# Performance work log

Measured on AMD Instinct MI355X. Metric: run time of the kernel, lower is better.

Reference implementation:

```python
import jax, jax.numpy as jnp
import numpy as np

B, S, D_IN, D_H = 4, 2048, 1024, 1024

def setup_inputs() -> dict:
    key = jax.random.key(0)
    kx, kq, kk, kv = jax.random.split(key, 4)
    # nn.Linear default init: U(-1/sqrt(fan_in), 1/sqrt(fan_in)); stored as [out, in]
    bound = 1.0 / np.sqrt(D_IN)
    x = jax.random.normal(kx, (B, S, D_IN), dtype=jnp.float32)
    W_q = jax.random.uniform(kq, (D_H, D_IN), jnp.float32, -bound, bound)
    W_k = jax.random.uniform(kk, (D_H, D_IN), jnp.float32, -bound, bound)
    W_v = jax.random.uniform(kv, (D_H, D_IN), jnp.float32, -bound, bound)
    return {"x": x, "W_q": W_q, "W_k": W_k, "W_v": W_v}

def reference(x, W_q, W_k, W_v):
    # Q = x @ W_q.T, etc. (nn.Linear with bias=False)
    Q = jnp.einsum('bsd,hd->bsh', x, W_q)
    K = jnp.einsum('bsd,hd->bsh', x, W_k)
    V = jnp.einsum('bsd,hd->bsh', x, W_v)
    # NOTE: original scales by sqrt(Q.shape[1]) == sqrt(seq_len), not sqrt(d)
    scale = 1.0 / jnp.sqrt(jnp.asarray(Q.shape[1], Q.dtype))
    scores = jnp.einsum('bqh,bkh->bqk', Q, K) * scale  # [B,S,S]
    attn = jax.nn.softmax(scores, axis=-1)
    return jnp.einsum('bqk,bkh->bqh', attn, V)
```

## Files before the change

kernel.cpp:

```cpp
#include <hip/hip_runtime.h>

typedef unsigned short ushort_t;
typedef __attribute__((ext_vector_type(8))) __bf16 bf16x8;
typedef __attribute__((ext_vector_type(4))) float floatx4;

__device__ __forceinline__ ushort_t f2bf(float f) {
    unsigned int u = __builtin_bit_cast(unsigned int, f);
    u = (u + 0x7fffu + ((u >> 16) & 1u)) >> 16;
    return (ushort_t)u;
}

__device__ __forceinline__ int sw(int row, int cg) {
    return ((row << 2) + ((cg ^ row ^ (row >> 2)) & 3)) << 3;
}

template <int BM, int BN, int IM, int IN>
__device__ __forceinline__ void gemm_core_pf(
    const ushort_t* __restrict__ A, int lda,
    const ushort_t* __restrict__ B, int ldb,
    int K, int tile_m, int tile_n,
    ushort_t* As, ushort_t* Bs,
    floatx4 (&acc)[IM][IN]) {

    constexpr int SA = BM * 4 / 256;
    constexpr int SB = BN * 4 / 256;

    const int tid  = threadIdx.x;
    const int lane = tid & 63;
    const int wave = tid >> 6;
    const int wm   = wave >> 1, wn = wave & 1;
    const int quad = lane >> 4;
    const int l16  = lane & 15;

#pragma unroll
    for (int i = 0; i < IM; i++)
#pragma unroll
        for (int j = 0; j < IN; j++) acc[i][j] = (floatx4){0.f, 0.f, 0.f, 0.f};

    const ushort_t* ga[SA];
    int la[SA];
#pragma unroll
    for (int s = 0; s < SA; s++) {
        int seg = tid + s * 256;
        int r = seg >> 2, c = (seg ^ r ^ (r >> 2)) & 3;
        ga[s] = A + (long)(r + tile_m) * lda + c * 8;
        la[s] = seg * 8;
    }
    const ushort_t* gb[SB];
    int lb[SB];
#pragma unroll
    for (int s = 0; s < SB; s++) {
        int seg = tid + s * 256;
        int r = seg >> 2, c = (seg ^ r ^ (r >> 2)) & 3;
        gb[s] = B + (long)(r + tile_n) * ldb + c * 8;
        lb[s] = seg * 8;
    }

    const int nk = K >> 5;

    bf16x8 ra[SA], rb[SB];
#pragma unroll
    for (int s = 0; s < SA; s++) ra[s] = *(const bf16x8*)ga[s];
#pragma unroll
    for (int s = 0; s < SB; s++) rb[s] = *(const bf16x8*)gb[s];
#pragma unroll
    for (int s = 0; s < SA; s++) *(bf16x8*)&As[la[s]] = ra[s];
#pragma unroll
    for (int s = 0; s < SB; s++) *(bf16x8*)&Bs[lb[s]] = rb[s];
    __syncthreads();

    for (int ks = 0; ks < nk; ++ks) {
        const int cur = ks & 1, nxt = cur ^ 1;

        if (ks + 1 < nk) {
            const int k1 = (ks + 1) << 5;
#pragma unroll
            for (int s = 0; s < SA; s++) ra[s] = *(const bf16x8*)(ga[s] + k1);
#pragma unroll
            for (int s = 0; s < SB; s++) rb[s] = *(const bf16x8*)(gb[s] + k1);
        }

        const ushort_t* as = &As[cur * BM * 32];
        const ushort_t* bs = &Bs[cur * BN * 32];
        bf16x8 af[IM], bfr[IN];
#pragma unroll
        for (int im = 0; im < IM; im++)
            af[im] = *(const bf16x8*)&as[sw(wm * IM * 16 + im * 16 + l16, quad)];
#pragma unroll
        for (int in = 0; in < IN; in++)
            bfr[in] = *(const bf16x8*)&bs[sw(wn * IN * 16 + in * 16 + l16, quad)];
#pragma unroll
        for (int im = 0; im < IM; im++)
#pragma unroll
            for (int in = 0; in < IN; in++)
                acc[im][in] = __builtin_amdgcn_mfma_f32_16x16x32_bf16(
                    af[im], bfr[in], acc[im][in], 0, 0, 0);

        if (ks + 1 < nk) {
#pragma unroll
            for (int s = 0; s < SA; s++) *(bf16x8*)&As[nxt * BM * 32 + la[s]] = ra[s];
#pragma unroll
            for (int s = 0; s < SB; s++) *(bf16x8*)&Bs[nxt * BN * 32 + lb[s]] = rb[s];
            __syncthreads();
        }
    }
}

__global__ void cvt_kernel(const float* __restrict__ x,
                           const float* __restrict__ wv,
                           ushort_t* __restrict__ xb,
                           ushort_t* __restrict__ wvb,
                           float* __restrict__ lsum) {
    const int bx = blockIdx.x;
    if (bx >= 9216) {
        int idx = (bx - 9216) * 256 + threadIdx.x;
        ((float4*)lsum)[idx] = (float4){0.f, 0.f, 0.f, 0.f};
        return;
    }
    const float* src;
    ushort_t* dst;
    long g;
    if (bx < 8192) { src = x;  dst = xb;  g = ((long)bx * 256 + threadIdx.x) * 4; }
    else           { src = wv; dst = wvb; g = ((long)(bx - 8192) * 256 + threadIdx.x) * 4; }
    float4 v = *(const float4*)(src + g);
    ushort4 o;
    o.x = f2bf(v.x); o.y = f2bf(v.y); o.z = f2bf(v.z); o.w = f2bf(v.w);
    *(ushort4*)(dst + g) = o;
}

__global__ void tkern(const float* __restrict__ wq, const float* __restrict__ wk,
                      ushort_t* __restrict__ wqT, ushort_t* __restrict__ wkT) {
    const float* src = blockIdx.z ? wk : wq;
    ushort_t* dst = blockIdx.z ? wkT : wqT;
    __shared__ ushort_t tile[64 * 80];

    const int t = threadIdx.x;
    const int h0 = blockIdx.y * 64, d0 = blockIdx.x * 64;
    {
        int i = t >> 2, cg = (t & 3) << 4;
        const float4* p = (const float4*)(src + (long)(h0 + i) * 1024 + d0 + cg);
#pragma unroll
        for (int k = 0; k < 4; k++) {
            float4 v = p[k];
            ushort_t* q = &tile[i * 80 + cg + k * 4];
            q[0] = f2bf(v.x); q[1] = f2bf(v.y); q[2] = f2bf(v.z); q[3] = f2bf(v.w);
        }
    }
    __syncthreads();
    {
        int j = t >> 2, ig = (t & 3) << 4;
        ushort_t tmp[16];
#pragma unroll
        for (int k = 0; k < 16; k++) tmp[k] = tile[(ig + k) * 80 + j];
        ushort_t* o = dst + (long)(d0 + j) * 1024 + h0 + ig;
        *(uint4*)o = ((uint4*)tmp)[0];
        *(uint4*)(o + 8) = ((uint4*)tmp)[1];
    }
}

__global__ __launch_bounds__(256) void ggemm_kernel(
    const ushort_t* __restrict__ wkT, const ushort_t* __restrict__ wqT,
    ushort_t* __restrict__ G) {
    __shared__ __align__(16) ushort_t As[2 * 64 * 32];
    __shared__ __align__(16) ushort_t Bs[2 * 64 * 32];
    const int tile_m = blockIdx.y * 64, tile_n = blockIdx.x * 64;
    floatx4 acc[2][2];
    gemm_core_pf<64, 64, 2, 2>(wkT, 1024, wqT, 1024, 1024, tile_m, tile_n, As, Bs, acc);
    const int lane = threadIdx.x & 63, wave = threadIdx.x >> 6;
    const int wm = wave >> 1, wn = wave & 1, quad = lane >> 4, l16 = lane & 15;
#pragma unroll
    for (int im = 0; im < 2; im++)
#pragma unroll
        for (int r = 0; r < 4; r++) {
            int row = tile_m + wm * 32 + im * 16 + quad * 4 + r;
#pragma unroll
            for (int in = 0; in < 2; in++) {
                int col = tile_n + wn * 32 + in * 16 + l16;
                G[(long)row * 1024 + col] = f2bf(acc[im][in][r]);
            }
        }
}

__global__ __launch_bounds__(256) void yv_kernel(
    const ushort_t* __restrict__ xb,
    const ushort_t* __restrict__ Gb,
    const ushort_t* __restrict__ wvb,
    ushort_t* __restrict__ Yb,
    ushort_t* __restrict__ VTb) {

    __shared__ __align__(16) ushort_t As[2 * 128 * 32];
    __shared__ __align__(16) ushort_t Bs[2 * 128 * 32];

    const int z = blockIdx.z;
    const ushort_t *A, *B;
    ushort_t* C;
    int ldc, tile_m, tile_n;
    if (z == 0) {
        A = xb; B = Gb; C = Yb; ldc = 1024;
        tile_m = blockIdx.y * 128; tile_n = blockIdx.x * 128;
    } else {
        A = wvb; B = xb; C = VTb; ldc = 8192;
        tile_m = blockIdx.x * 128; tile_n = blockIdx.y * 128;
    }

    floatx4 acc[4][4];
    gemm_core_pf<128, 128, 4, 4>(A, 1024, B, 1024, 1024, tile_m, tile_n, As, Bs, acc);

    const int lane = threadIdx.x & 63, wave = threadIdx.x >> 6;
    const int wm = wave >> 1, wn = wave & 1, quad = lane >> 4, l16 = lane & 15;
#pragma unroll
    for (int im = 0; im < 4; im++)
#pragma unroll
        for (int r = 0; r < 4; r++) {
            int row = tile_m + wm * 64 + im * 16 + quad * 4 + r;
#pragma unroll
            for (int in = 0; in < 4; in++) {
                int col = tile_n + wn * 64 + in * 16 + l16;
                C[(long)row * ldc + col] = f2bf(acc[im][in][r]);
            }
        }
}

__global__ __launch_bounds__(256) void pexp_kernel(
    const ushort_t* __restrict__ Yb,
    const ushort_t* __restrict__ xb,
    ushort_t* __restrict__ Pb,
    float* __restrict__ lsum) {

    __shared__ __align__(16) ushort_t As[2 * 128 * 32];
    __shared__ __align__(16) ushort_t Bs[2 * 128 * 32];

    const int z = blockIdx.z;
    const ushort_t* A = Yb + (long)z * 2097152;
    const ushort_t* B = xb + (long)z * 2097152;
    ushort_t* C = Pb + (long)z * 4194304;
    float* l = lsum + z * 2048;
    const int tile_m = blockIdx.y * 128;
    const int tile_n = blockIdx.x * 128;

    floatx4 acc[4][4];
    gemm_core_pf<128, 128, 4, 4>(A, 1024, B, 1024, 1024, tile_m, tile_n, As, Bs, acc);

    const float scale = 0.022097086912079608f;
    const int lane = threadIdx.x & 63, wave = threadIdx.x >> 6;
    const int wm = wave >> 1, wn = wave & 1, quad = lane >> 4, l16 = lane & 15;
#pragma unroll
    for (int im = 0; im < 4; im++)
#pragma unroll
        for (int r = 0; r < 4; r++) {
            int row = tile_m + wm * 64 + im * 16 + quad * 4 + r;
            float psum = 0.f;
#pragma unroll
            for (int in = 0; in < 4; in++) {
                int col = tile_n + wn * 64 + in * 16 + l16;
                float e = __expf(acc[im][in][r] * scale);
                C[(long)row * 2048 + col] = f2bf(e);
                psum += e;
            }
            psum += __shfl_xor(psum, 1, 64);
            psum += __shfl_xor(psum, 2, 64);
            psum += __shfl_xor(psum, 4, 64);
            psum += __shfl_xor(psum, 8, 64);
            if (l16 == 0) atomicAdd(&l[row], psum);
        }
}

__global__ __launch_bounds__(256) void out_kernel(
    const ushort_t* __restrict__ Pb,
    const ushort_t* __restrict__ VTb,
    float* __restrict__ out,
    const float* __restrict__ lsum) {

    __shared__ __align__(16) ushort_t As[2 * 128 * 32];
    __shared__ __align__(16) ushort_t Bs[2 * 128 * 32];

    const int z = blockIdx.z;
    const ushort_t* A = Pb + (long)z * 4194304;
    const ushort_t* B = VTb + (long)z * 2048;
    float* C = out + (long)z * 2097152;
    const float* l = lsum + z * 2048;
    const int tile_m = blockIdx.y * 128;
    const int tile_n = blockIdx.x * 128;

    floatx4 acc[4][4];
    gemm_core_pf<128, 128, 4, 4>(A, 2048, B, 8192, 2048, tile_m, tile_n, As, Bs, acc);

    const int lane = threadIdx.x & 63, wave = threadIdx.x >> 6;
    const int wm = wave >> 1, wn = wave & 1, quad = lane >> 4, l16 = lane & 15;
#pragma unroll
    for (int im = 0; im < 4; im++)
#pragma unroll
        for (int r = 0; r < 4; r++) {
            int row = tile_m + wm * 64 + im * 16 + quad * 4 + r;
            float li = 1.0f / l[row];
#pragma unroll
            for (int in = 0; in < 4; in++) {
                int col = tile_n + wn * 64 + in * 16 + l16;
                C[(long)row * 1024 + col] = acc[im][in][r] * li;
            }
        }
}

extern "C" void kernel_launch(void* const* d_in, const int* in_sizes, int n_in,
                              void* d_out, int out_size, void* d_ws, size_t ws_size,
                              hipStream_t stream) {
    const float* x  = (const float*)d_in[0];
    const float* wq = (const float*)d_in[1];
    const float* wk = (const float*)d_in[2];
    const float* wv = (const float*)d_in[3];

    ushort_t* xb  = (ushort_t*)d_ws;
    ushort_t* wvb = xb  + 8388608;
    ushort_t* wqT = wvb + 1048576;
    ushort_t* wkT = wqT + 1048576;
    ushort_t* Gb  = wkT + 1048576;
    ushort_t* Yb  = Gb  + 1048576;
    ushort_t* VTb = Yb  + 8388608;
    ushort_t* Pb  = VTb + 8388608;
    float*    lsum = (float*)(Pb + 16777216);
    float*    out  = (float*)d_out;

    cvt_kernel<<<9224, 256, 0, stream>>>(x, wv, xb, wvb, lsum);

    tkern<<<dim3(16, 16, 2), 256, 0, stream>>>(wq, wk, wqT, wkT);

    ggemm_kernel<<<dim3(16, 16), 256, 0, stream>>>(wkT, wqT, Gb);

    yv_kernel<<<dim3(8, 64, 2), 256, 0, stream>>>(xb, Gb, wvb, Yb, VTb);

    pexp_kernel<<<dim3(16, 16, 4), 256, 0, stream>>>(Yb, xb, Pb, lsum);

    out_kernel<<<dim3(8, 16, 4), 256, 0, stream>>>(Pb, VTb, out, lsum);
}
```

Measured before the change: 269.8 us.

## Use async global-to-LDS loads with triple-buffered pipeline in GEMM core

Replaces the register-staged double-buffered GEMM main loop with direct global_load_lds async copies into a three-slot shared buffer, prefetching two k-steps ahead. The wait on outstanding loads uses explicit vmcnt counts plus a barrier. The aim is to remove the register round trip and the VGPRs used for staging, and to hide more load latency. In exchange it uses more LDS per block (48KB for the 128-tile kernels), which may lower occupancy. It also depends on hand-tuned vmcnt counts being correct.

```diff
diff --git a/kernel.cpp b/kernel.cpp
--- a/kernel.cpp
+++ b/kernel.cpp
@@ -10,20 +10,29 @@
     return (ushort_t)u;
 }
 
+__device__ __forceinline__ void async16(const ushort_t* g, ushort_t* l) {
+    __builtin_amdgcn_global_load_lds(
+        (const __attribute__((address_space(1))) unsigned int*)g,
+        (__attribute__((address_space(3))) unsigned int*)l,
+        16 , 0 , 0 );
+}
+
 __device__ __forceinline__ int sw(int row, int cg) {
     return ((row << 2) + ((cg ^ row ^ (row >> 2)) & 3)) << 3;
 }
 
 template <int BM, int BN, int IM, int IN>
-__device__ __forceinline__ void gemm_core_pf(
+__device__ __forceinline__ void gemm_core_p3(
     const ushort_t* __restrict__ A, int lda,
     const ushort_t* __restrict__ B, int ldb,
     int K, int tile_m, int tile_n,
-    ushort_t* As, ushort_t* Bs,
+    ushort_t* buf,
     floatx4 (&acc)[IM][IN]) {
 
     constexpr int SA = BM * 4 / 256;
     constexpr int SB = BN * 4 / 256;
+    constexpr int SLOT = (BM + BN) * 32;
+    constexpr int BOFF = BM * 32;
 
     const int tid  = threadIdx.x;
     const int lane = tid & 63;
@@ -53,35 +62,43 @@
         int seg = tid + s * 256;
         int r = seg >> 2, c = (seg ^ r ^ (r >> 2)) & 3;
         gb[s] = B + (long)(r + tile_n) * ldb + c * 8;
-        lb[s] = seg * 8;
+        lb[s] = BOFF + seg * 8;
     }
 
     const int nk = K >> 5;
 
-    bf16x8 ra[SA], rb[SB];
-#pragma unroll
-    for (int s = 0; s < SA; s++) ra[s] = *(const bf16x8*)ga[s];
-#pragma unroll
-    for (int s = 0; s < SB; s++) rb[s] = *(const bf16x8*)gb[s];
-#pragma unroll
-    for (int s = 0; s < SA; s++) *(bf16x8*)&As[la[s]] = ra[s];
-#pragma unroll
-    for (int s = 0; s < SB; s++) *(bf16x8*)&Bs[lb[s]] = rb[s];
-    __syncthreads();
-
-    for (int ks = 0; ks < nk; ++ks) {
-        const int cur = ks & 1, nxt = cur ^ 1;
-
-        if (ks + 1 < nk) {
-            const int k1 = (ks + 1) << 5;
-#pragma unroll
-            for (int s = 0; s < SA; s++) ra[s] = *(const bf16x8*)(ga[s] + k1);
-#pragma unroll
-            for (int s = 0; s < SB; s++) rb[s] = *(const bf16x8*)(gb[s] + k1);
-        }
-
-        const ushort_t* as = &As[cur * BM * 32];
-        const ushort_t* bs = &Bs[cur * BN * 32];
+#pragma unroll
+    for (int p = 0; p < 2; ++p) {
+#pragma unroll
+        for (int s = 0; s < SA; s++) async16(ga[s] + p * 32, buf + p * SLOT + la[s]);
+#pragma unroll
+        for (int s = 0; s < SB; s++) async16(gb[s] + p * 32, buf + p * SLOT + lb[s]);
+    }
+
+    int slot = 0, slot2 = 2;
+    for (int k = 0; k < nk; ++k) {
+        if (k + 1 < nk) {
+            if constexpr (SA + SB == 4)
+                asm volatile("s_waitcnt vmcnt(4)" ::: "memory");
+            else
+                asm volatile("s_waitcnt vmcnt(2)" ::: "memory");
+        } else {
+            asm volatile("s_waitcnt vmcnt(0)" ::: "memory");
+        }
+        __builtin_amdgcn_s_barrier();
+        asm volatile("" ::: "memory");
+
+        if (k + 2 < nk) {
+            const int koff = (k + 2) << 5;
+            ushort_t* dst = buf + slot2 * SLOT;
+#pragma unroll
+            for (int s = 0; s < SA; s++) async16(ga[s] + koff, dst + la[s]);
+#pragma unroll
+            for (int s = 0; s < SB; s++) async16(gb[s] + koff, dst + lb[s]);
+        }
+
+        const ushort_t* as = buf + slot * SLOT;
+        const ushort_t* bs = as + BOFF;
         bf16x8 af[IM], bfr[IN];
 #pragma unroll
         for (int im = 0; im < IM; im++)
@@ -96,13 +113,8 @@
                 acc[im][in] = __builtin_amdgcn_mfma_f32_16x16x32_bf16(
                     af[im], bfr[in], acc[im][in], 0, 0, 0);
 
-        if (ks + 1 < nk) {
-#pragma unroll
-            for (int s = 0; s < SA; s++) *(bf16x8*)&As[nxt * BM * 32 + la[s]] = ra[s];
-#pragma unroll
-            for (int s = 0; s < SB; s++) *(bf16x8*)&Bs[nxt * BN * 32 + lb[s]] = rb[s];
-            __syncthreads();
-        }
+        slot  = (slot == 2) ? 0 : slot + 1;
+        slot2 = (slot2 == 2) ? 0 : slot2 + 1;
     }
 }
 
@@ -161,11 +173,10 @@
 __global__ __launch_bounds__(256) void ggemm_kernel(
     const ushort_t* __restrict__ wkT, const ushort_t* __restrict__ wqT,
     ushort_t* __restrict__ G) {
-    __shared__ __align__(16) ushort_t As[2 * 64 * 32];
-    __shared__ __align__(16) ushort_t Bs[2 * 64 * 32];
+    __shared__ __align__(16) ushort_t buf[3 * 128 * 32];
     const int tile_m = blockIdx.y * 64, tile_n = blockIdx.x * 64;
     floatx4 acc[2][2];
-    gemm_core_pf<64, 64, 2, 2>(wkT, 1024, wqT, 1024, 1024, tile_m, tile_n, As, Bs, acc);
+    gemm_core_p3<64, 64, 2, 2>(wkT, 1024, wqT, 1024, 1024, tile_m, tile_n, buf, acc);
     const int lane = threadIdx.x & 63, wave = threadIdx.x >> 6;
     const int wm = wave >> 1, wn = wave & 1, quad = lane >> 4, l16 = lane & 15;
 #pragma unroll
@@ -188,8 +199,7 @@
     ushort_t* __restrict__ Yb,
     ushort_t* __restrict__ VTb) {
 
-    __shared__ __align__(16) ushort_t As[2 * 128 * 32];
-    __shared__ __align__(16) ushort_t Bs[2 * 128 * 32];
+    __shared__ __align__(16) ushort_t buf[3 * 256 * 32];
 
     const int z = blockIdx.z;
     const ushort_t *A, *B;
@@ -204,7 +214,7 @@
     }
 
     floatx4 acc[4][4];
-    gemm_core_pf<128, 128, 4, 4>(A, 1024, B, 1024, 1024, tile_m, tile_n, As, Bs, acc);
+    gemm_core_p3<128, 128, 4, 4>(A, 1024, B, 1024, 1024, tile_m, tile_n, buf, acc);
 
     const int lane = threadIdx.x & 63, wave = threadIdx.x >> 6;
     const int wm = wave >> 1, wn = wave & 1, quad = lane >> 4, l16 = lane & 15;
@@ -227,8 +237,7 @@
     ushort_t* __restrict__ Pb,
     float* __restrict__ lsum) {
 
-    __shared__ __align__(16) ushort_t As[2 * 128 * 32];
-    __shared__ __align__(16) ushort_t Bs[2 * 128 * 32];
+    __shared__ __align__(16) ushort_t buf[3 * 256 * 32];
 
     const int z = blockIdx.z;
     const ushort_t* A = Yb + (long)z * 2097152;
@@ -239,7 +248,7 @@
     const int tile_n = blockIdx.x * 128;
 
     floatx4 acc[4][4];
-    gemm_core_pf<128, 128, 4, 4>(A, 1024, B, 1024, 1024, tile_m, tile_n, As, Bs, acc);
+    gemm_core_p3<128, 128, 4, 4>(A, 1024, B, 1024, 1024, tile_m, tile_n, buf, acc);
 
     const float scale = 0.022097086912079608f;
     const int lane = threadIdx.x & 63, wave = threadIdx.x >> 6;
@@ -271,8 +280,7 @@
     float* __restrict__ out,
     const float* __restrict__ lsum) {
 
-    __shared__ __align__(16) ushort_t As[2 * 128 * 32];
-    __shared__ __align__(16) ushort_t Bs[2 * 128 * 32];
+    __shared__ __align__(16) ushort_t buf[3 * 256 * 32];
 
     const int z = blockIdx.z;
     const ushort_t* A = Pb + (long)z * 4194304;
@@ -283,7 +291,7 @@
     const int tile_n = blockIdx.x * 128;
 
     floatx4 acc[4][4];
-    gemm_core_pf<128, 128, 4, 4>(A, 2048, B, 8192, 2048, tile_m, tile_n, As, Bs, acc);
+    gemm_core_p3<128, 128, 4, 4>(A, 2048, B, 8192, 2048, tile_m, tile_n, buf, acc);
 
     const int lane = threadIdx.x & 63, wave = threadIdx.x >> 6;
     const int wm = wave >> 1, wn = wave & 1, quad = lane >> 4, l16 = lane & 15;
```

Result: faster. 243.9 us (-9.6%).
